# Kernel optimization log

Hardware: AMD Instinct MI355X
Metric: run time of the kernel (lower is better)

## Reference

```python
import jax, jax.numpy as jnp
import numpy as np

N = 200_000        # atoms
E = 800_000        # directed edges (pairs e, e^1 are mutual reverses)
H = 512            # hidden_size
AF = 133           # atom_feat_size
BF = 14            # bond_feat_size
B = 4096           # num graphs


def setup_inputs() -> dict:
    key = jax.random.key(0)
    ks = jax.random.split(key, 8)
    atom_hiddens = jax.random.normal(ks[0], (N, H), dtype=jnp.float32)
    # undirected bonds, then interleave as (src,dst),(dst,src) so rev[e] = e ^ 1
    src = jax.random.randint(ks[1], (E // 2,), 0, N, dtype=jnp.int32)
    dst = jax.random.randint(ks[2], (E // 2,), 0, N, dtype=jnp.int32)
    heads = jnp.stack([src, dst], axis=1).reshape(-1)   # [E]
    tails = jnp.stack([dst, src], axis=1).reshape(-1)   # [E]
    edge_index = jnp.stack([heads, tails], axis=0)      # [2, E]
    rev_edge_index = jnp.arange(E, dtype=jnp.int32) ^ 1
    batch = jnp.sort(jax.random.randint(ks[3], (N,), 0, B, dtype=jnp.int32))
    batch = batch.at[-1].set(B - 1)  # batch[-1]+1 == B, matching the torch code
    s = 1.0 / np.sqrt(H)
    return {
        "atom_hiddens": atom_hiddens,
        "W_node": jax.random.normal(ks[4], (H, AF), dtype=jnp.float32) * s,
        "b_node": jnp.zeros((AF,), dtype=jnp.float32),
        "W_edge": jax.random.normal(ks[5], (H, BF), dtype=jnp.float32) * s,
        "b_edge": jnp.zeros((BF,), dtype=jnp.float32),
        "W_g1": jax.random.normal(ks[6], (H, H), dtype=jnp.float32) * s,
        "b_g1": jnp.zeros((H,), dtype=jnp.float32),
        "W_g2": jax.random.normal(ks[7], (H, 1), dtype=jnp.float32) * s,
        "b_g2": jnp.zeros((1,), dtype=jnp.float32),
        "edge_index": edge_index,
        "rev_edge_index": rev_edge_index,
        "batch": batch,
        "num_graphs": B,
    }


def reference(atom_hiddens, W_node, b_node, W_edge, b_edge, W_g1, b_g1,
              W_g2, b_g2, edge_index, rev_edge_index, batch, num_graphs):
    # graph pooling: index_add_ over the sorted batch vector
    graph_emb = jax.ops.segment_sum(atom_hiddens, batch, num_segments=num_graphs)
    # node head
    node_pred = atom_hiddens @ W_node + b_node
    # edge dedup: the torch loop keeps edge e iff its reverse was not yet
    # visited, i.e. iff e < rev_edge_index[e] (rev is an involution), giving
    # exactly E//2 kept edges.
    e_ids = jnp.arange(edge_index.shape[1])
    keep = jnp.nonzero(e_ids < rev_edge_index, size=edge_index.shape[1] // 2,
                       fill_value=0)[0]
    a1 = edge_index[0, keep]
    a2 = edge_index[1, keep]
    bond_emb = 0.5 * (atom_hiddens[a1] + atom_hiddens[a2])  # [E//2, H]
    edge_pred = bond_emb @ W_edge + b_edge
    # graph head: Linear -> ReLU -> Linear
    graph_pred = jax.nn.relu(graph_emb @ W_g1 + b_g1) @ W_g2 + b_g2
    return node_pred, edge_pred, graph_pred
```

## Files before the change

### kernel.cpp

```cpp
#include <hip/hip_runtime.h>

#define NATOMS 200000
#define NEDGE  800000
#define NBOND  400000
#define HDIM   512
#define AF     133
#define BFEAT  14
#define NGRAPH 4096

#define NODE_OUT_SZ (NATOMS * AF)
#define EDGE_OUT_SZ (NBOND * BFEAT)

#define WS_P     0
#define WS_BMAT  12800000
#define WS_BIAS  12963840
#define WS_GEF   12964480
#define WS_WG1T  21353088

typedef _Float16 half8 __attribute__((ext_vector_type(8)));
typedef float floatx4 __attribute__((ext_vector_type(4)));

__global__ void pack_kernel(const float* __restrict__ Wn, const float* __restrict__ bn,
                            const float* __restrict__ We, const float* __restrict__ be,
                            const float* __restrict__ Wg1, const float* __restrict__ bg2,
                            _Float16* __restrict__ Bmat, float* __restrict__ bias,
                            _Float16* __restrict__ Wg1t, float* __restrict__ gpred) {
    int idx = blockIdx.x * 256 + threadIdx.x;
    if (idx < 160 * 512) {
        int n = idx >> 9, k = idx & 511;
        float v = 0.f;
        if (n < AF)              v = Wn[k * AF + n];
        else if (n < AF + BFEAT) v = We[k * BFEAT + (n - AF)];
        Bmat[idx] = (_Float16)v;
    } else if (idx < 160 * 512 + 512 * 512) {
        int i = idx - 160 * 512;
        int n = i >> 9, k = i & 511;
        Wg1t[i] = (_Float16)Wg1[k * HDIM + n];
    } else if (idx < 160 * 512 + 512 * 512 + 160) {
        int n = idx - (160 * 512 + 512 * 512);
        float v = 0.f;
        if (n < AF)              v = bn[n];
        else if (n < AF + BFEAT) v = be[n - AF];
        bias[n] = v;
    } else if (idx < 160 * 512 + 512 * 512 + 160 + NGRAPH) {
        gpred[idx - (160 * 512 + 512 * 512 + 160)] = bg2[0];
    }
}

__global__ void zero_ge(float4* __restrict__ GEf4) {
    GEf4[blockIdx.x * 256 + threadIdx.x] = make_float4(0.f, 0.f, 0.f, 0.f);
}

__global__ __launch_bounds__(256) void gemm_node(const float* __restrict__ A,
                                                 const _Float16* __restrict__ Bm,
                                                 const float* __restrict__ bias,
                                                 const int* __restrict__ batch,
                                                 float* __restrict__ node_out,
                                                 float* __restrict__ P,
                                                 float* __restrict__ GEf) {
    __shared__ _Float16 As[128][72];
    __shared__ _Float16 Bs[160][72];
    __shared__ int bg[128];

    const int t    = threadIdx.x;
    const int bm   = blockIdx.x;
    const int w    = t >> 6, l = t & 63, quad = l >> 4, lr = l & 15;
    const int wm   = w & 1, wn = w >> 1;

    if (t < 128) {
        int grow = bm * 128 + t;
        bg[t] = (grow < NATOMS) ? batch[grow] : -1;
    }

    floatx4 acc[4][5];
    for (int mt = 0; mt < 4; ++mt)
        for (int nt = 0; nt < 5; ++nt)
            acc[mt][nt] = (floatx4){0.f, 0.f, 0.f, 0.f};

    const int arow0 = t >> 2;
    const int aseg  = (t & 3) * 16;
    const int pc    = t & 63;
    const int pq    = w;

    for (int ko = 0; ko < 8; ++ko) {
        const int k0 = ko * 64;
        float4 av[2][4];
        for (int p = 0; p < 2; ++p) {
            int row = arow0 + p * 64;
            long grow = (long)bm * 128 + row;
            if (grow < NATOMS) {
                const float4* src = (const float4*)(A + grow * HDIM + k0 + aseg);
                av[p][0] = src[0]; av[p][1] = src[1]; av[p][2] = src[2]; av[p][3] = src[3];
            } else {
                av[p][0] = av[p][1] = av[p][2] = av[p][3] = make_float4(0.f, 0.f, 0.f, 0.f);
            }
        }
        uint4 bv[5];
        for (int it = 0; it < 5; ++it) {
            int idx = t + it * 256;
            int row = idx >> 3, c = (idx & 7) * 8;
            bv[it] = *(const uint4*)(Bm + row * HDIM + k0 + c);
        }
        __syncthreads();
        for (int p = 0; p < 2; ++p) {
            int row = arow0 + p * 64;
            half8 h0 = {(_Float16)av[p][0].x, (_Float16)av[p][0].y, (_Float16)av[p][0].z, (_Float16)av[p][0].w,
                        (_Float16)av[p][1].x, (_Float16)av[p][1].y, (_Float16)av[p][1].z, (_Float16)av[p][1].w};
            half8 h1 = {(_Float16)av[p][2].x, (_Float16)av[p][2].y, (_Float16)av[p][2].z, (_Float16)av[p][2].w,
                        (_Float16)av[p][3].x, (_Float16)av[p][3].y, (_Float16)av[p][3].z, (_Float16)av[p][3].w};
            *(half8*)&As[row][aseg]     = h0;
            *(half8*)&As[row][aseg + 8] = h1;
        }
        for (int it = 0; it < 5; ++it) {
            int idx = t + it * 256;
            int row = idx >> 3, c = (idx & 7) * 8;
            *(uint4*)&Bs[row][c] = bv[it];
        }
        __syncthreads();
        for (int kk = 0; kk < 64; kk += 32) {
            half8 af[4], bf[5];
            for (int mt = 0; mt < 4; ++mt)
                af[mt] = *(const half8*)&As[wm * 64 + mt * 16 + lr][kk + quad * 8];
            for (int nt = 0; nt < 5; ++nt)
                bf[nt] = *(const half8*)&Bs[wn * 80 + nt * 16 + lr][kk + quad * 8];
            for (int mt = 0; mt < 4; ++mt)
                for (int nt = 0; nt < 5; ++nt)
                    acc[mt][nt] = __builtin_amdgcn_mfma_f32_16x16x32_f16(af[mt], bf[nt], acc[mt][nt], 0, 0, 0);
        }
        {
            float psum = 0.f;
            int pg = bg[pq * 32];
            for (int r = pq * 32; r < pq * 32 + 32; ++r) {
                int gid = bg[r];
                if (gid != pg) {
                    if (pg >= 0) atomicAdd(&GEf[(size_t)pg * HDIM + k0 + pc], psum);
                    psum = 0.f; pg = gid;
                }
                psum += (float)As[r][pc];
            }
            if (pg >= 0) atomicAdd(&GEf[(size_t)pg * HDIM + k0 + pc], psum);
        }
    }

    float biasv[5];
    for (int nt = 0; nt < 5; ++nt) biasv[nt] = bias[wn * 80 + nt * 16 + lr];
    for (int mt = 0; mt < 4; ++mt) {
        int rbase = bm * 128 + wm * 64 + mt * 16 + quad * 4;
        for (int r = 0; r < 4; ++r) {
            int grow = rbase + r;
            if (grow >= NATOMS) continue;
            for (int nt = 0; nt < 5; ++nt) {
                int gcol = wn * 80 + nt * 16 + lr;
                float v = acc[mt][nt][r] + biasv[nt];
                if (gcol < AF)                  node_out[(long)grow * AF + gcol] = v;
                else if (gcol < AF + BFEAT)     P[(long)grow * 16 + (gcol - AF)] = v;
            }
        }
    }
}

__global__ __launch_bounds__(256) void edge_kernel(const int* __restrict__ ei,
                                                   const float* __restrict__ P,
                                                   float* __restrict__ eout) {
    int t  = threadIdx.x;
    int j  = t & 15, bi = t >> 4;
    int b  = blockIdx.x * 16 + bi;
    if (b >= NBOND) return;
    if (j < BFEAT) {
        int e  = 2 * b;
        int a1 = ei[e];
        int a2 = ei[NEDGE + e];
        float v = 0.5f * (P[(size_t)a1 * 16 + j] + P[(size_t)a2 * 16 + j]);
        eout[(size_t)b * BFEAT + j] = v;
    }
}

__global__ __launch_bounds__(256) void gemm_graph(const float* __restrict__ GEf,
                                                  const _Float16* __restrict__ Bt,
                                                  const float* __restrict__ bg1,
                                                  const float* __restrict__ wg2,
                                                  float* __restrict__ gpred) {
    __shared__ _Float16 As[128][72];
    __shared__ _Float16 Bs[128][72];

    const int t   = threadIdx.x;
    const int bmb = blockIdx.x, bnb = blockIdx.y;
    const int w   = t >> 6, l = t & 63, quad = l >> 4, lr = l & 15;
    const int wm  = w & 1, wn = w >> 1;

    floatx4 acc[4][4];
    for (int mt = 0; mt < 4; ++mt)
        for (int nt = 0; nt < 4; ++nt)
            acc[mt][nt] = (floatx4){0.f, 0.f, 0.f, 0.f};

    const int arow0 = t >> 2;
    const int aseg  = (t & 3) * 16;

    for (int ko = 0; ko < 8; ++ko) {
        const int k0 = ko * 64;
        float4 av[2][4];
        for (int p = 0; p < 2; ++p) {
            int row = bmb * 128 + arow0 + p * 64;
            const float4* src = (const float4*)(GEf + (size_t)row * HDIM + k0 + aseg);
            av[p][0] = src[0]; av[p][1] = src[1]; av[p][2] = src[2]; av[p][3] = src[3];
        }
        uint4 bvv[4];
        for (int it = 0; it < 4; ++it) {
            int idx = t + it * 256;
            int row = idx >> 3, c = (idx & 7) * 8;
            bvv[it] = *(const uint4*)(Bt + (size_t)(bnb * 128 + row) * HDIM + k0 + c);
        }
        __syncthreads();
        for (int p = 0; p < 2; ++p) {
            int row = arow0 + p * 64;
            half8 h0 = {(_Float16)av[p][0].x, (_Float16)av[p][0].y, (_Float16)av[p][0].z, (_Float16)av[p][0].w,
                        (_Float16)av[p][1].x, (_Float16)av[p][1].y, (_Float16)av[p][1].z, (_Float16)av[p][1].w};
            half8 h1 = {(_Float16)av[p][2].x, (_Float16)av[p][2].y, (_Float16)av[p][2].z, (_Float16)av[p][2].w,
                        (_Float16)av[p][3].x, (_Float16)av[p][3].y, (_Float16)av[p][3].z, (_Float16)av[p][3].w};
            *(half8*)&As[row][aseg]     = h0;
            *(half8*)&As[row][aseg + 8] = h1;
        }
        for (int it = 0; it < 4; ++it) {
            int idx = t + it * 256;
            int row = idx >> 3, c = (idx & 7) * 8;
            *(uint4*)&Bs[row][c] = bvv[it];
        }
        __syncthreads();
        for (int kk = 0; kk < 64; kk += 32) {
            half8 af[4], bf[4];
            for (int mt = 0; mt < 4; ++mt)
                af[mt] = *(const half8*)&As[wm * 64 + mt * 16 + lr][kk + quad * 8];
            for (int nt = 0; nt < 4; ++nt)
                bf[nt] = *(const half8*)&Bs[wn * 64 + nt * 16 + lr][kk + quad * 8];
            for (int mt = 0; mt < 4; ++mt)
                for (int nt = 0; nt < 4; ++nt)
                    acc[mt][nt] = __builtin_amdgcn_mfma_f32_16x16x32_f16(af[mt], bf[nt], acc[mt][nt], 0, 0, 0);
        }
    }

    float bg1v[4], wg2v[4];
    for (int nt = 0; nt < 4; ++nt) {
        int col = bnb * 128 + wn * 64 + nt * 16 + lr;
        bg1v[nt] = bg1[col];
        wg2v[nt] = wg2[col];
    }
    for (int mt = 0; mt < 4; ++mt) {
        for (int r = 0; r < 4; ++r) {
            int row = bmb * 128 + wm * 64 + mt * 16 + quad * 4 + r;
            float partial = 0.f;
            for (int nt = 0; nt < 4; ++nt) {
                float v = acc[mt][nt][r] + bg1v[nt];
                v = v > 0.f ? v : 0.f;
                partial += v * wg2v[nt];
            }
            partial += __shfl_xor(partial, 1);
            partial += __shfl_xor(partial, 2);
            partial += __shfl_xor(partial, 4);
            partial += __shfl_xor(partial, 8);
            if (lr == 0) atomicAdd(&gpred[row], partial);
        }
    }
}

extern "C" void kernel_launch(void* const* d_in, const int* in_sizes, int n_in,
                              void* d_out, int out_size, void* d_ws, size_t ws_size,
                              hipStream_t stream) {
    const float* A    = (const float*)d_in[0];
    const float* Wn   = (const float*)d_in[1];
    const float* bn   = (const float*)d_in[2];
    const float* We   = (const float*)d_in[3];
    const float* be   = (const float*)d_in[4];
    const float* Wg1  = (const float*)d_in[5];
    const float* bg1  = (const float*)d_in[6];
    const float* Wg2  = (const float*)d_in[7];
    const float* bg2  = (const float*)d_in[8];
    const int*   ei   = (const int*)d_in[9];
    const int*   batch= (const int*)d_in[11];

    char* ws = (char*)d_ws;
    float*    P    = (float*)(ws + WS_P);
    _Float16* Bmat = (_Float16*)(ws + WS_BMAT);
    float*    bias = (float*)(ws + WS_BIAS);
    float*    GEf  = (float*)(ws + WS_GEF);
    _Float16* Wg1t = (_Float16*)(ws + WS_WG1T);

    float* node_out = (float*)d_out;
    float* edge_out = node_out + NODE_OUT_SZ;
    float* gpred    = edge_out + EDGE_OUT_SZ;

    pack_kernel<<<dim3(1361), dim3(256), 0, stream>>>(Wn, bn, We, be, Wg1, bg2, Bmat, bias, Wg1t, gpred);
    zero_ge<<<dim3(NGRAPH * HDIM / 4 / 256), dim3(256), 0, stream>>>((float4*)GEf);
    gemm_node<<<dim3((NATOMS + 127) / 128), dim3(256), 0, stream>>>(A, Bmat, bias, batch, node_out, P, GEf);
    edge_kernel<<<dim3(NBOND / 16), dim3(256), 0, stream>>>(ei, P, edge_out);
    gemm_graph<<<dim3(32, 4), dim3(256), 0, stream>>>(GEf, Wg1t, bg1, Wg2, gpred);
}
```

Measured before the change: 747.0 us.

## Double-buffer A tile, read B fragments from global, vectorize edge kernel

The node GEMM now double-buffers the A tile in shared memory and prefetches the next K tile into registers while the current one feeds the MFMAs. The B shared-memory tile is dropped and B fragments are loaded straight from global/L2, which removes one barrier per iteration. Launch bounds now request three waves per SIMD, and loops are explicitly unrolled. The edge kernel uses float4 gathers with four threads per bond instead of sixteen scalar threads, at the cost of more register pressure and redundant global B reads across waves.

```diff
diff --git a/kernel.cpp b/kernel.cpp
--- a/kernel.cpp
+++ b/kernel.cpp
@@ -51,15 +51,14 @@
     GEf4[blockIdx.x * 256 + threadIdx.x] = make_float4(0.f, 0.f, 0.f, 0.f);
 }
 
-__global__ __launch_bounds__(256) void gemm_node(const float* __restrict__ A,
-                                                 const _Float16* __restrict__ Bm,
-                                                 const float* __restrict__ bias,
-                                                 const int* __restrict__ batch,
-                                                 float* __restrict__ node_out,
-                                                 float* __restrict__ P,
-                                                 float* __restrict__ GEf) {
-    __shared__ _Float16 As[128][72];
-    __shared__ _Float16 Bs[160][72];
+__global__ __launch_bounds__(256, 3) void gemm_node(const float* __restrict__ A,
+                                                    const _Float16* __restrict__ Bm,
+                                                    const float* __restrict__ bias,
+                                                    const int* __restrict__ batch,
+                                                    float* __restrict__ node_out,
+                                                    float* __restrict__ P,
+                                                    float* __restrict__ GEf) {
+    __shared__ _Float16 As[2][128][72];
     __shared__ int bg[128];
 
     const int t    = threadIdx.x;
@@ -73,7 +72,9 @@
     }
 
     floatx4 acc[4][5];
+#pragma unroll
     for (int mt = 0; mt < 4; ++mt)
+#pragma unroll
         for (int nt = 0; nt < 5; ++nt)
             acc[mt][nt] = (floatx4){0.f, 0.f, 0.f, 0.f};
 
@@ -82,12 +83,17 @@
     const int pc    = t & 63;
     const int pq    = w;
 
-    for (int ko = 0; ko < 8; ++ko) {
+    int boff[5];
+#pragma unroll
+    for (int nt = 0; nt < 5; ++nt)
+        boff[nt] = (wn * 80 + nt * 16 + lr) * HDIM + quad * 8;
+
+    float4 av[2][4];
+    auto load_tile = [&](int ko) {
         const int k0 = ko * 64;
-        float4 av[2][4];
+#pragma unroll
         for (int p = 0; p < 2; ++p) {
-            int row = arow0 + p * 64;
-            long grow = (long)bm * 128 + row;
+            long grow = (long)bm * 128 + arow0 + p * 64;
             if (grow < NATOMS) {
                 const float4* src = (const float4*)(A + grow * HDIM + k0 + aseg);
                 av[p][0] = src[0]; av[p][1] = src[1]; av[p][2] = src[2]; av[p][3] = src[3];
@@ -95,60 +101,95 @@
                 av[p][0] = av[p][1] = av[p][2] = av[p][3] = make_float4(0.f, 0.f, 0.f, 0.f);
             }
         }
-        uint4 bv[5];
-        for (int it = 0; it < 5; ++it) {
-            int idx = t + it * 256;
-            int row = idx >> 3, c = (idx & 7) * 8;
-            bv[it] = *(const uint4*)(Bm + row * HDIM + k0 + c);
-        }
-        __syncthreads();
+    };
+    auto cvt_store = [&](int buf) {
+#pragma unroll
         for (int p = 0; p < 2; ++p) {
             int row = arow0 + p * 64;
             half8 h0 = {(_Float16)av[p][0].x, (_Float16)av[p][0].y, (_Float16)av[p][0].z, (_Float16)av[p][0].w,
                         (_Float16)av[p][1].x, (_Float16)av[p][1].y, (_Float16)av[p][1].z, (_Float16)av[p][1].w};
             half8 h1 = {(_Float16)av[p][2].x, (_Float16)av[p][2].y, (_Float16)av[p][2].z, (_Float16)av[p][2].w,
                         (_Float16)av[p][3].x, (_Float16)av[p][3].y, (_Float16)av[p][3].z, (_Float16)av[p][3].w};
-            *(half8*)&As[row][aseg]     = h0;
-            *(half8*)&As[row][aseg + 8] = h1;
-        }
-        for (int it = 0; it < 5; ++it) {
-            int idx = t + it * 256;
-            int row = idx >> 3, c = (idx & 7) * 8;
-            *(uint4*)&Bs[row][c] = bv[it];
-        }
-        __syncthreads();
-        for (int kk = 0; kk < 64; kk += 32) {
-            half8 af[4], bf[5];
-            for (int mt = 0; mt < 4; ++mt)
-                af[mt] = *(const half8*)&As[wm * 64 + mt * 16 + lr][kk + quad * 8];
-            for (int nt = 0; nt < 5; ++nt)
-                bf[nt] = *(const half8*)&Bs[wn * 80 + nt * 16 + lr][kk + quad * 8];
-            for (int mt = 0; mt < 4; ++mt)
+            *(half8*)&As[buf][row][aseg]     = h0;
+            *(half8*)&As[buf][row][aseg + 8] = h1;
+        }
+    };
+
+    load_tile(0);
+    cvt_store(0);
+    __syncthreads();
+
+    for (int ko = 0; ko < 8; ++ko) {
+        const int k0  = ko * 64;
+        const int cur = ko & 1;
+
+        half8 bfa[5], bfb[5];
+#pragma unroll
+        for (int nt = 0; nt < 5; ++nt) bfa[nt] = *(const half8*)(Bm + boff[nt] + k0);
+#pragma unroll
+        for (int nt = 0; nt < 5; ++nt) bfb[nt] = *(const half8*)(Bm + boff[nt] + k0 + 32);
+        if (ko < 7) load_tile(ko + 1);
+
+        {
+            half8 af[4];
+#pragma unroll
+            for (int mt = 0; mt < 4; ++mt)
+                af[mt] = *(const half8*)&As[cur][wm * 64 + mt * 16 + lr][quad * 8];
+#pragma unroll
+            for (int mt = 0; mt < 4; ++mt)
+#pragma unroll
                 for (int nt = 0; nt < 5; ++nt)
-                    acc[mt][nt] = __builtin_amdgcn_mfma_f32_16x16x32_f16(af[mt], bf[nt], acc[mt][nt], 0, 0, 0);
-        }
+                    acc[mt][nt] = __builtin_amdgcn_mfma_f32_16x16x32_f16(af[mt], bfa[nt], acc[mt][nt], 0, 0, 0);
+#pragma unroll
+            for (int mt = 0; mt < 4; ++mt)
+                af[mt] = *(const half8*)&As[cur][wm * 64 + mt * 16 + lr][32 + quad * 8];
+#pragma unroll
+            for (int mt = 0; mt < 4; ++mt)
+#pragma unroll
+                for (int nt = 0; nt < 5; ++nt)
+                    acc[mt][nt] = __builtin_amdgcn_mfma_f32_16x16x32_f16(af[mt], bfb[nt], acc[mt][nt], 0, 0, 0);
+        }
+
         {
             float psum = 0.f;
             int pg = bg[pq * 32];
-            for (int r = pq * 32; r < pq * 32 + 32; ++r) {
-                int gid = bg[r];
-                if (gid != pg) {
-                    if (pg >= 0) atomicAdd(&GEf[(size_t)pg * HDIM + k0 + pc], psum);
-                    psum = 0.f; pg = gid;
+#pragma unroll
+            for (int rb = 0; rb < 32; rb += 8) {
+                float vals[8];
+#pragma unroll
+                for (int i = 0; i < 8; ++i)
+                    vals[i] = (float)As[cur][pq * 32 + rb + i][pc];
+#pragma unroll
+                for (int i = 0; i < 8; ++i) {
+                    int r = pq * 32 + rb + i;
+                    int gid = bg[r];
+                    if (gid != pg) {
+                        if (pg >= 0) atomicAdd(&GEf[(size_t)pg * HDIM + k0 + pc], psum);
+                        psum = 0.f; pg = gid;
+                    }
+                    psum += vals[i];
                 }
-                psum += (float)As[r][pc];
             }
             if (pg >= 0) atomicAdd(&GEf[(size_t)pg * HDIM + k0 + pc], psum);
         }
+
+        if (ko < 7) {
+            cvt_store(cur ^ 1);
+            __syncthreads();
+        }
     }
 
     float biasv[5];
+#pragma unroll
     for (int nt = 0; nt < 5; ++nt) biasv[nt] = bias[wn * 80 + nt * 16 + lr];
+#pragma unroll
     for (int mt = 0; mt < 4; ++mt) {
         int rbase = bm * 128 + wm * 64 + mt * 16 + quad * 4;
+#pragma unroll
         for (int r = 0; r < 4; ++r) {
             int grow = rbase + r;
             if (grow >= NATOMS) continue;
+#pragma unroll
             for (int nt = 0; nt < 5; ++nt) {
                 int gcol = wn * 80 + nt * 16 + lr;
                 float v = acc[mt][nt][r] + biasv[nt];
@@ -163,16 +204,21 @@
                                                    const float* __restrict__ P,
                                                    float* __restrict__ eout) {
     int t  = threadIdx.x;
-    int j  = t & 15, bi = t >> 4;
-    int b  = blockIdx.x * 16 + bi;
+    int q  = t & 3, bi = t >> 2;
+    int b  = blockIdx.x * 64 + bi;
     if (b >= NBOND) return;
-    if (j < BFEAT) {
-        int e  = 2 * b;
-        int a1 = ei[e];
-        int a2 = ei[NEDGE + e];
-        float v = 0.5f * (P[(size_t)a1 * 16 + j] + P[(size_t)a2 * 16 + j]);
-        eout[(size_t)b * BFEAT + j] = v;
-    }
+    int e  = 2 * b;
+    int a1 = ei[e];
+    int a2 = ei[NEDGE + e];
+    const float4 v1 = *(const float4*)(P + (size_t)a1 * 16 + q * 4);
+    const float4 v2 = *(const float4*)(P + (size_t)a2 * 16 + q * 4);
+    float r[4] = {0.5f * (v1.x + v2.x), 0.5f * (v1.y + v2.y),
+                  0.5f * (v1.z + v2.z), 0.5f * (v1.w + v2.w)};
+    float* dst = eout + (size_t)b * BFEAT + q * 4;
+    int rem = BFEAT - q * 4;
+#pragma unroll
+    for (int i = 0; i < 4; ++i)
+        if (i < rem) dst[i] = r[i];
 }
 
 __global__ __launch_bounds__(256) void gemm_graph(const float* __restrict__ GEf,
@@ -291,6 +337,6 @@
     pack_kernel<<<dim3(1361), dim3(256), 0, stream>>>(Wn, bn, We, be, Wg1, bg2, Bmat, bias, Wg1t, gpred);
     zero_ge<<<dim3(NGRAPH * HDIM / 4 / 256), dim3(256), 0, stream>>>((float4*)GEf);
     gemm_node<<<dim3((NATOMS + 127) / 128), dim3(256), 0, stream>>>(A, Bmat, bias, batch, node_out, P, GEf);
-    edge_kernel<<<dim3(NBOND / 16), dim3(256), 0, stream>>>(ei, P, edge_out);
+    edge_kernel<<<dim3((NBOND + 63) / 64), dim3(256), 0, stream>>>(ei, P, edge_out);
     gemm_graph<<<dim3(32, 4), dim3(256), 0, stream>>>(GEf, Wg1t, bg1, Wg2, gpred);
 }
```

Result: slower. 801.3 us (+7.3%).
